# Kernel optimization log

Measured on AMD Instinct MI355X. Metric: run time of the kernel, lower is better.

## Reference

```python
import jax, jax.numpy as jnp
import numpy as np
from jax import lax


def _transform_points(pts, M, eps=1e-8):
    # pytorch3d row-vector convention: p' = [p, 1] @ M, then perspective divide by w.
    ph = jnp.concatenate([pts, jnp.ones(pts.shape[:-1] + (1,), pts.dtype)], axis=-1)
    out = jnp.einsum('bnk,bkl->bnl', ph, M)
    w = out[..., 3:4]
    w = jnp.where(jnp.abs(w) < eps, eps, w)
    return out[..., :3] / w


def _rasterize_spheres(pts_screen, radius, image_size, K):
    # pts_screen: [B,N,3] with (x,y) in NDC and z = view-space depth; radius: [B,N].
    # Per pixel: keep K front-most (smallest z>0) points with NDC dist2 <= radius^2.
    B, N, _ = pts_screen.shape
    half = 1.0 - 1.0 / image_size
    coords = jnp.linspace(half, -half, image_size, dtype=pts_screen.dtype)  # pytorch3d NDC: +x left, +y up
    py, px = jnp.meshgrid(coords, coords, indexing='ij')  # [H,W]
    dx = pts_screen[:, None, None, :, 0] - px[None, :, :, None]  # [B,H,W,N]
    dy = pts_screen[:, None, None, :, 1] - py[None, :, :, None]
    dist2 = dx * dx + dy * dy
    z = pts_screen[:, None, None, :, 2]  # [B,1,1,N]
    inside = (dist2 <= (radius * radius)[:, None, None, :]) & (z > 0)
    zmask = jnp.where(inside, z, jnp.inf)
    negz, inds = lax.top_k(-zmask, K)  # K smallest z (front-most) per pixel
    valid = jnp.isfinite(negz)
    zbuf = jnp.where(valid, -negz, jnp.float32(-1.0))
    d2 = jnp.take_along_axis(dist2, inds, axis=-1)
    dists = jnp.where(valid, d2, jnp.float32(-1.0))
    idx = jnp.where(valid, inds, -1)
    return idx, zbuf, dists


def setup_inputs() -> dict:
    key = jax.random.key(0)
    k1, k2 = jax.random.split(key)
    B, N = 1, 1024
    points = jax.random.normal(k1, (B, N, 3), dtype=jnp.float32)
    radius = 0.02 + 0.06 * jax.random.uniform(k2, (B, N), dtype=jnp.float32)
    # Rigid world->view: identity rotation, translate camera so points sit at z ~ 3 (row-vector convention).
    w2v = np.eye(4, dtype=np.float32)
    w2v[3, 2] = 3.0
    world2view = jnp.asarray(w2v)[None]
    # Perspective projection (row-vector): [x,y,z,1] @ P = [s x, s y, a z + b, z]
    s, znear, zfar = 2.0, 0.1, 100.0
    a = zfar / (zfar - znear)
    b = -zfar * znear / (zfar - znear)
    proj = jnp.asarray(np.array([[s, 0, 0, 0], [0, s, 0, 0], [0, 0, a, 1], [0, 0, b, 0]], dtype=np.float32))[None]
    return {'points': points, 'radius': radius, 'world2view': world2view, 'proj': proj,
            'image_size': 256, 'points_per_pixel': 8}


def reference(points, radius, world2view, proj, image_size, points_per_pixel):
    pts_view = _transform_points(points, world2view)
    pts_screen = _transform_points(pts_view, proj)
    pts_screen = pts_screen.at[..., 2].set(pts_view[..., 2])  # keep view-space depth
    idx, zbuf, dists = _rasterize_spheres(pts_screen, radius, image_size, points_per_pixel)
    return idx, zbuf, dists
```

## Files before the change

kernel.cpp:

```cpp
#include <hip/hip_runtime.h>
#include <math.h>


#define KPP 8

__global__ __launch_bounds__(256) void sphere_raster_kernel(
    const float* __restrict__ points,
    const float* __restrict__ radius,
    const float* __restrict__ w2v,
    const float* __restrict__ proj,
    float* __restrict__ out,
    int B, int N, int H, int W)
{
    extern __shared__ char smem[];
    float4* cmp  = (float4*)smem;
    int*    cidx = (int*)(smem + (size_t)N * sizeof(float4));
    __shared__ int wsum[4];

    const int TS = 16;
    const int tilesX = W / TS;
    const int tile   = blockIdx.x % (tilesX * (H / TS));
    const int b      = blockIdx.x / (tilesX * (H / TS));
    const int tx0    = (tile % tilesX) * TS;
    const int ty0    = (tile / tilesX) * TS;
    const int j      = tx0 + (threadIdx.x & (TS - 1));
    const int i      = ty0 + (threadIdx.x >> 4);
    const int lane   = threadIdx.x & 63;
    const int wid    = threadIdx.x >> 6;

    const float* M1 = w2v  + (size_t)b * 16;
    const float* M2 = proj + (size_t)b * 16;

    const double halfd = 1.0 - 1.0 / (double)W;
    const double step  = 2.0 * halfd / (double)(W - 1);
    const float px = (float)(halfd - (double)j * step);
    const float py = (float)(halfd - (double)i * step);

    const float cx = (float)(halfd - ((double)tx0 + (TS - 1) * 0.5) * step);
    const float cy = (float)(halfd - ((double)ty0 + (TS - 1) * 0.5) * step);
    const float hext = (float)(((TS - 1) * 0.5 + 1.0) * step);

    const int t0 = threadIdx.x * 4;
    float4 P[4];
    int keep[4];
    int c = 0;

    const float4* pv = (const float4*)(points + ((size_t)b * N + t0) * 3);
    float4 q0 = pv[0], q1 = pv[1], q2 = pv[2];
    float4 rr = *(const float4*)(radius + (size_t)b * N + t0);
    float xs[4] = {q0.x, q0.w, q1.z, q2.y};
    float ys[4] = {q0.y, q1.x, q1.w, q2.z};
    float zs[4] = {q0.z, q1.y, q2.x, q2.w};
    float rv[4] = {rr.x, rr.y, rr.z, rr.w};

#pragma unroll
    for (int s = 0; s < 4; ++s) {
        float x = xs[s], y = ys[s], z = zs[s];
        float vx = ((x * M1[0] + y * M1[4]) + z * M1[8])  + M1[12];
        float vy = ((x * M1[1] + y * M1[5]) + z * M1[9])  + M1[13];
        float vz = ((x * M1[2] + y * M1[6]) + z * M1[10]) + M1[14];
        float vw = ((x * M1[3] + y * M1[7]) + z * M1[11]) + M1[15];
        float w1 = (fabsf(vw) < 1e-8f) ? 1e-8f : vw;
        vx /= w1; vy /= w1; vz /= w1;
        float sx = ((vx * M2[0] + vy * M2[4]) + vz * M2[8])  + M2[12];
        float sy = ((vx * M2[1] + vy * M2[5]) + vz * M2[9])  + M2[13];
        float sw = ((vx * M2[3] + vy * M2[7]) + vz * M2[11]) + M2[15];
        float w2 = (fabsf(sw) < 1e-8f) ? 1e-8f : sw;
        sx /= w2; sy /= w2;
        float r = rv[s];
        float r2eff = (vz > 0.0f) ? r * r : -1.0f;
        float dxm = fmaxf(0.0f, fabsf(sx - cx) - hext);
        float dym = fmaxf(0.0f, fabsf(sy - cy) - hext);
        float dmin2 = dxm * dxm + dym * dym;
        keep[s] = (dmin2 <= r2eff + 1e-6f) ? 1 : 0;
        P[s] = make_float4(sx, sy, vz, r2eff);
        c += keep[s];
    }

    int pre = c;
#pragma unroll
    for (int d = 1; d < 64; d <<= 1) {
        int v = __shfl_up(pre, d);
        if (lane >= d) pre += v;
    }
    if (lane == 63) wsum[wid] = pre;
    __syncthreads();
    int wbase = 0, M = 0;
#pragma unroll
    for (int w = 0; w < 4; ++w) {
        int ws = wsum[w];
        if (w < wid) wbase += ws;
        M += ws;
    }
    int pos = wbase + (pre - c);
#pragma unroll
    for (int s = 0; s < 4; ++s) {
        if (keep[s]) { cmp[pos] = P[s]; cidx[pos] = t0 + s; ++pos; }
    }
    __syncthreads();

    float zb[KPP]; int id[KPP]; float dd[KPP];
#pragma unroll
    for (int k = 0; k < KPP; ++k) { zb[k] = INFINITY; id[k] = -1; dd[k] = -1.0f; }

    int n = 0;
    for (; n + 8 <= M; n += 8) {
        float4 pp[8];
#pragma unroll
        for (int u = 0; u < 8; ++u) pp[u] = cmp[n + u];
        int4 ia = *(const int4*)&cidx[n];
        int4 ib = *(const int4*)&cidx[n + 4];
        int ii[8] = {ia.x, ia.y, ia.z, ia.w, ib.x, ib.y, ib.z, ib.w};
#pragma unroll
        for (int u = 0; u < 8; ++u) {
            float dx = pp[u].x - px;
            float dy = pp[u].y - py;
            float dist2 = __fadd_rn(__fmul_rn(dx, dx), __fmul_rn(dy, dy));
            if ((dist2 <= pp[u].w) && (pp[u].z < zb[KPP - 1])) {
                float zc = pp[u].z; int ic = ii[u]; float dc = dist2;
#pragma unroll
                for (int k = 0; k < KPP; ++k) {
                    bool lt = (zc < zb[k]);
                    float tz = zb[k]; int ti = id[k]; float td = dd[k];
                    if (lt) { zb[k] = zc; id[k] = ic; dd[k] = dc; zc = tz; ic = ti; dc = td; }
                }
            }
        }
    }
    for (; n < M; ++n) {
        float4 p = cmp[n];
        int ic0 = cidx[n];
        float dx = p.x - px;
        float dy = p.y - py;
        float dist2 = __fadd_rn(__fmul_rn(dx, dx), __fmul_rn(dy, dy));
        if ((dist2 <= p.w) && (p.z < zb[KPP - 1])) {
            float zc = p.z; int ic = ic0; float dc = dist2;
#pragma unroll
            for (int k = 0; k < KPP; ++k) {
                bool lt = (zc < zb[k]);
                float tz = zb[k]; int ti = id[k]; float td = dd[k];
                if (lt) { zb[k] = zc; id[k] = ic; dd[k] = dc; zc = tz; ic = ti; dc = td; }
            }
        }
    }

    const size_t pix   = ((size_t)b * H + i) * W + j;
    const size_t plane = (size_t)B * H * W * KPP;
    float vidx[KPP], vzbf[KPP], vdst[KPP];
#pragma unroll
    for (int k = 0; k < KPP; ++k) {
        bool valid = (zb[k] != INFINITY);
        vidx[k] = valid ? (float)id[k] : -1.0f;
        vzbf[k] = valid ? zb[k]        : -1.0f;
        vdst[k] = valid ? dd[k]        : -1.0f;
    }
    float* oidx = out + pix * KPP;
    float* ozbf = out + plane + pix * KPP;
    float* odst = out + 2 * plane + pix * KPP;
    *(float4*)(oidx)     = make_float4(vidx[0], vidx[1], vidx[2], vidx[3]);
    *(float4*)(oidx + 4) = make_float4(vidx[4], vidx[5], vidx[6], vidx[7]);
    *(float4*)(ozbf)     = make_float4(vzbf[0], vzbf[1], vzbf[2], vzbf[3]);
    *(float4*)(ozbf + 4) = make_float4(vzbf[4], vzbf[5], vzbf[6], vzbf[7]);
    *(float4*)(odst)     = make_float4(vdst[0], vdst[1], vdst[2], vdst[3]);
    *(float4*)(odst + 4) = make_float4(vdst[4], vdst[5], vdst[6], vdst[7]);
}

extern "C" void kernel_launch(void* const* d_in, const int* in_sizes, int n_in,
                              void* d_out, int out_size, void* d_ws, size_t ws_size,
                              hipStream_t stream) {
    const float* points = (const float*)d_in[0];
    const float* radius = (const float*)d_in[1];
    const float* w2v    = (const float*)d_in[2];
    const float* proj   = (const float*)d_in[3];
    int B = in_sizes[2] / 16;
    if (B < 1) B = 1;
    int N = in_sizes[1] / B;
    int HW = out_size / (3 * B * KPP);
    int H = 1;
    while ((H + 1) * (H + 1) <= HW) ++H;
    int W = H;

    int tiles = (W / 16) * (H / 16);
    dim3 grid(B * tiles);
    dim3 block(256);
    size_t shmem = (size_t)N * (sizeof(float4) + sizeof(int));
    sphere_raster_kernel<<<grid, block, shmem, stream>>>(
        points, radius, w2v, proj, (float*)d_out, B, N, H, W);
}
```

Measured before the change: 14.70 us.

## Precompute point transforms in a separate kernel and broadcast candidates via readlane

Moves the per-point world-to-screen transform out of the raster kernel into a small pre-kernel that writes float4 records to workspace. Before, every tile block recomputed the transform for all points; now each point is transformed once. The raster inner loop also changes: each wave loads 64 candidates into lanes once and broadcasts them with readlane instead of every thread reading shared memory. This costs an extra kernel launch and a global round trip, and the readlane loop is no longer unrolled.

```diff
diff --git a/kernel.cpp b/kernel.cpp
--- a/kernel.cpp
+++ b/kernel.cpp
@@ -4,11 +4,40 @@
 
 #define KPP 8
 
-__global__ __launch_bounds__(256) void sphere_raster_kernel(
+__global__ __launch_bounds__(256) void transform_kernel(
     const float* __restrict__ points,
     const float* __restrict__ radius,
     const float* __restrict__ w2v,
     const float* __restrict__ proj,
+    float4* __restrict__ ws,
+    int B, int N)
+{
+    int t = blockIdx.x * blockDim.x + threadIdx.x;
+    if (t >= B * N) return;
+    int b = t / N;
+    const float* M1 = w2v  + (size_t)b * 16;
+    const float* M2 = proj + (size_t)b * 16;
+    float x = points[(size_t)t * 3 + 0];
+    float y = points[(size_t)t * 3 + 1];
+    float z = points[(size_t)t * 3 + 2];
+    float vx = ((x * M1[0] + y * M1[4]) + z * M1[8])  + M1[12];
+    float vy = ((x * M1[1] + y * M1[5]) + z * M1[9])  + M1[13];
+    float vz = ((x * M1[2] + y * M1[6]) + z * M1[10]) + M1[14];
+    float vw = ((x * M1[3] + y * M1[7]) + z * M1[11]) + M1[15];
+    float w1 = (fabsf(vw) < 1e-8f) ? 1e-8f : vw;
+    vx /= w1; vy /= w1; vz /= w1;
+    float sx = ((vx * M2[0] + vy * M2[4]) + vz * M2[8])  + M2[12];
+    float sy = ((vx * M2[1] + vy * M2[5]) + vz * M2[9])  + M2[13];
+    float sw = ((vx * M2[3] + vy * M2[7]) + vz * M2[11]) + M2[15];
+    float w2 = (fabsf(sw) < 1e-8f) ? 1e-8f : sw;
+    sx /= w2; sy /= w2;
+    float r = radius[t];
+    float r2eff = (vz > 0.0f) ? r * r : -1.0f;
+    ws[t] = make_float4(sx, sy, vz, r2eff);
+}
+
+__global__ __launch_bounds__(256) void sphere_raster_kernel(
+    const float4* __restrict__ ws,
     float* __restrict__ out,
     int B, int N, int H, int W)
 {
@@ -28,9 +57,6 @@
     const int lane   = threadIdx.x & 63;
     const int wid    = threadIdx.x >> 6;
 
-    const float* M1 = w2v  + (size_t)b * 16;
-    const float* M2 = proj + (size_t)b * 16;
-
     const double halfd = 1.0 - 1.0 / (double)W;
     const double step  = 2.0 * halfd / (double)(W - 1);
     const float px = (float)(halfd - (double)j * step);
@@ -41,39 +67,18 @@
     const float hext = (float)(((TS - 1) * 0.5 + 1.0) * step);
 
     const int t0 = threadIdx.x * 4;
+    const float4* base4 = ws + (size_t)b * N + t0;
     float4 P[4];
     int keep[4];
     int c = 0;
-
-    const float4* pv = (const float4*)(points + ((size_t)b * N + t0) * 3);
-    float4 q0 = pv[0], q1 = pv[1], q2 = pv[2];
-    float4 rr = *(const float4*)(radius + (size_t)b * N + t0);
-    float xs[4] = {q0.x, q0.w, q1.z, q2.y};
-    float ys[4] = {q0.y, q1.x, q1.w, q2.z};
-    float zs[4] = {q0.z, q1.y, q2.x, q2.w};
-    float rv[4] = {rr.x, rr.y, rr.z, rr.w};
-
 #pragma unroll
     for (int s = 0; s < 4; ++s) {
-        float x = xs[s], y = ys[s], z = zs[s];
-        float vx = ((x * M1[0] + y * M1[4]) + z * M1[8])  + M1[12];
-        float vy = ((x * M1[1] + y * M1[5]) + z * M1[9])  + M1[13];
-        float vz = ((x * M1[2] + y * M1[6]) + z * M1[10]) + M1[14];
-        float vw = ((x * M1[3] + y * M1[7]) + z * M1[11]) + M1[15];
-        float w1 = (fabsf(vw) < 1e-8f) ? 1e-8f : vw;
-        vx /= w1; vy /= w1; vz /= w1;
-        float sx = ((vx * M2[0] + vy * M2[4]) + vz * M2[8])  + M2[12];
-        float sy = ((vx * M2[1] + vy * M2[5]) + vz * M2[9])  + M2[13];
-        float sw = ((vx * M2[3] + vy * M2[7]) + vz * M2[11]) + M2[15];
-        float w2 = (fabsf(sw) < 1e-8f) ? 1e-8f : sw;
-        sx /= w2; sy /= w2;
-        float r = rv[s];
-        float r2eff = (vz > 0.0f) ? r * r : -1.0f;
-        float dxm = fmaxf(0.0f, fabsf(sx - cx) - hext);
-        float dym = fmaxf(0.0f, fabsf(sy - cy) - hext);
+        float4 p = base4[s];
+        float dxm = fmaxf(0.0f, fabsf(p.x - cx) - hext);
+        float dym = fmaxf(0.0f, fabsf(p.y - cy) - hext);
         float dmin2 = dxm * dxm + dym * dym;
-        keep[s] = (dmin2 <= r2eff + 1e-6f) ? 1 : 0;
-        P[s] = make_float4(sx, sy, vz, r2eff);
+        keep[s] = (dmin2 <= p.w + 1e-6f) ? 1 : 0;
+        P[s] = p;
         c += keep[s];
     }
 
@@ -88,9 +93,9 @@
     int wbase = 0, M = 0;
 #pragma unroll
     for (int w = 0; w < 4; ++w) {
-        int ws = wsum[w];
-        if (w < wid) wbase += ws;
-        M += ws;
+        int s = wsum[w];
+        if (w < wid) wbase += s;
+        M += s;
     }
     int pos = wbase + (pre - c);
 #pragma unroll
@@ -103,43 +108,30 @@
 #pragma unroll
     for (int k = 0; k < KPP; ++k) { zb[k] = INFINITY; id[k] = -1; dd[k] = -1.0f; }
 
-    int n = 0;
-    for (; n + 8 <= M; n += 8) {
-        float4 pp[8];
+    for (int bb = 0; bb < M; bb += 64) {
+        int li = bb + lane;
+        float4 pl;
+        int il;
+        if (li < M) { pl = cmp[li]; il = cidx[li]; }
+        else { pl = make_float4(0.0f, 0.0f, INFINITY, -1.0f); il = -1; }
+        int cnt = (M - bb < 64) ? (M - bb) : 64;
+        for (int k = 0; k < cnt; ++k) {
+            float sx = __int_as_float(__builtin_amdgcn_readlane(__float_as_int(pl.x), k));
+            float sy = __int_as_float(__builtin_amdgcn_readlane(__float_as_int(pl.y), k));
+            float sz = __int_as_float(__builtin_amdgcn_readlane(__float_as_int(pl.z), k));
+            float sw = __int_as_float(__builtin_amdgcn_readlane(__float_as_int(pl.w), k));
+            int   si = __builtin_amdgcn_readlane(il, k);
+            float dx = sx - px;
+            float dy = sy - py;
+            float dist2 = __fadd_rn(__fmul_rn(dx, dx), __fmul_rn(dy, dy));
+            if ((dist2 <= sw) && (sz < zb[KPP - 1])) {
+                float zc = sz; int ic = si; float dc = dist2;
 #pragma unroll
-        for (int u = 0; u < 8; ++u) pp[u] = cmp[n + u];
-        int4 ia = *(const int4*)&cidx[n];
-        int4 ib = *(const int4*)&cidx[n + 4];
-        int ii[8] = {ia.x, ia.y, ia.z, ia.w, ib.x, ib.y, ib.z, ib.w};
-#pragma unroll
-        for (int u = 0; u < 8; ++u) {
-            float dx = pp[u].x - px;
-            float dy = pp[u].y - py;
-            float dist2 = __fadd_rn(__fmul_rn(dx, dx), __fmul_rn(dy, dy));
-            if ((dist2 <= pp[u].w) && (pp[u].z < zb[KPP - 1])) {
-                float zc = pp[u].z; int ic = ii[u]; float dc = dist2;
-#pragma unroll
-                for (int k = 0; k < KPP; ++k) {
-                    bool lt = (zc < zb[k]);
-                    float tz = zb[k]; int ti = id[k]; float td = dd[k];
-                    if (lt) { zb[k] = zc; id[k] = ic; dd[k] = dc; zc = tz; ic = ti; dc = td; }
+                for (int k2 = 0; k2 < KPP; ++k2) {
+                    bool lt = (zc < zb[k2]);
+                    float tz = zb[k2]; int ti = id[k2]; float td = dd[k2];
+                    if (lt) { zb[k2] = zc; id[k2] = ic; dd[k2] = dc; zc = tz; ic = ti; dc = td; }
                 }
-            }
-        }
-    }
-    for (; n < M; ++n) {
-        float4 p = cmp[n];
-        int ic0 = cidx[n];
-        float dx = p.x - px;
-        float dy = p.y - py;
-        float dist2 = __fadd_rn(__fmul_rn(dx, dx), __fmul_rn(dy, dy));
-        if ((dist2 <= p.w) && (p.z < zb[KPP - 1])) {
-            float zc = p.z; int ic = ic0; float dc = dist2;
-#pragma unroll
-            for (int k = 0; k < KPP; ++k) {
-                bool lt = (zc < zb[k]);
-                float tz = zb[k]; int ti = id[k]; float td = dd[k];
-                if (lt) { zb[k] = zc; id[k] = ic; dd[k] = dc; zc = tz; ic = ti; dc = td; }
             }
         }
     }
@@ -180,10 +172,14 @@
     while ((H + 1) * (H + 1) <= HW) ++H;
     int W = H;
 
+    float4* ws = (float4*)d_ws;
+
+    int total = B * N;
+    transform_kernel<<<(total + 255) / 256, 256, 0, stream>>>(
+        points, radius, w2v, proj, ws, B, N);
+
     int tiles = (W / 16) * (H / 16);
-    dim3 grid(B * tiles);
-    dim3 block(256);
     size_t shmem = (size_t)N * (sizeof(float4) + sizeof(int));
-    sphere_raster_kernel<<<grid, block, shmem, stream>>>(
-        points, radius, w2v, proj, (float*)d_out, B, N, H, W);
+    sphere_raster_kernel<<<B * tiles, 256, shmem, stream>>>(
+        ws, (float*)d_out, B, N, H, W);
 }
```

Result: slower. 19.66 us (+33.7%).
